# Kernel optimization log

Measured on AMD Instinct MI355X. Metric: run time of the kernel, lower is better.

## Reference

```python
import jax, jax.numpy as jnp
import numpy as np

B, CIN, H, W = 16, 3, 224, 224
COUT = 128
EPS = 1e-5  # BatchNorm2d default eps


def setup_inputs() -> dict:
    key = jax.random.key(0)
    ks = jax.random.split(key, 7)
    x = jax.random.normal(ks[0], (B, CIN, H, W), dtype=jnp.float32)
    conv_w = jax.random.normal(ks[1], (COUT, CIN, 7, 7), dtype=jnp.float32) * 0.05
    conv_b = jax.random.normal(ks[2], (COUT,), dtype=jnp.float32) * 0.05
    bn_gamma = 1.0 + 0.1 * jax.random.normal(ks[3], (COUT,), dtype=jnp.float32)
    bn_beta = 0.05 * jax.random.normal(ks[4], (COUT,), dtype=jnp.float32)
    bn_mean = 0.1 * jax.random.normal(ks[5], (COUT,), dtype=jnp.float32)
    bn_var = jax.random.uniform(ks[6], (COUT,), dtype=jnp.float32, minval=0.5, maxval=1.5)
    return {"x": x, "conv_w": conv_w, "conv_b": conv_b, "bn_gamma": bn_gamma,
            "bn_beta": bn_beta, "bn_mean": bn_mean, "bn_var": bn_var}


def reference(x, conv_w, conv_b, bn_gamma, bn_beta, bn_mean, bn_var):
    b = x.shape[0]
    # Conv2d 3->128, k7, stride 1, pad 3  -> [B,128,H,W]
    y = jax.lax.conv_general_dilated(
        x, conv_w, window_strides=(1, 1), padding=[(3, 3), (3, 3)],
        dimension_numbers=("NCHW", "OIHW", "NCHW"))
    y = y + conv_b[None, :, None, None]
    # BatchNorm2d (inference form with running stats), then ReLU
    scale = bn_gamma * jax.lax.rsqrt(bn_var + EPS)
    y = (y - bn_mean[None, :, None, None]) * scale[None, :, None, None] + bn_beta[None, :, None, None]
    y = jax.nn.relu(y)
    h, w = y.shape[2], y.shape[3]
    # channel-last, top-3 over channels -> [B,H,W,3]
    y_cl = jnp.transpose(y, (0, 2, 3, 1))
    top3, idx3 = jax.lax.top_k(y_cl, 3)
    # MaxPool3d kernel (3,1,1) over the top-3 axis of [B,3,H,W]: max of the 3
    # sorted top-k values == top3[..., 0]. Flatten spatial -> [B,1,H*W]
    max_vals = top3[..., 0].reshape(b, 1, h * w)
    _, idx = jax.lax.top_k(max_vals, 128)  # idx: [B,1,128] flat spatial indices
    # flatten top3/idx3 to [B,3,H*W] (channel-first layout, matching torch transposes)
    top3_f = jnp.transpose(top3, (0, 3, 1, 2)).reshape(b, 3, h * w)
    idx3_f = jnp.transpose(idx3, (0, 3, 1, 2)).reshape(b, 3, h * w)
    gidx = jnp.broadcast_to(idx, (b, 3, 128))
    reduced_top3 = jnp.take_along_axis(top3_f, gidx, axis=2)              # [B,3,128]
    reduced_idx3 = jnp.take_along_axis(idx3_f, gidx, axis=2).astype(jnp.float32)
    return reduced_idx3, reduced_top3, idx
```

## Files before the change

kernel.cpp:

```cpp
#include <hip/hip_runtime.h>
#include <math.h>

#define BATCH 16
#define CIN   3
#define HH    224
#define WW    224
#define HW    (HH*WW)
#define COUT  128
#define TAPS  147
#define CAND  192
#define TK    192

typedef __attribute__((ext_vector_type(8))) _Float16 f16x8_t;
typedef decltype(__builtin_amdgcn_cvt_pkrtz(0.f, 0.f)) f16x2_t;
typedef __attribute__((ext_vector_type(4))) float f32x4_t;
typedef __attribute__((ext_vector_type(16))) float f32x16_t;
typedef __attribute__((ext_vector_type(4))) unsigned int u32x4_t;
typedef unsigned long long u64;
typedef unsigned int u32;

#define B_CHUNKS  (24*129)
#define B_BYTES   (B_CHUNKS*16u)
#define CPY_STRIDE 2192
#define CPY_BYTES  (8*CPY_STRIDE)
#define XFSTR     25
#define XF_OFF    (B_BYTES + CPY_BYTES)
#define LBSH_OFF  (XF_OFF + 6656u)
#define PMAX_OFF  (LBSH_OFF + 512u)
#define LHIST_OFF (PMAX_OFF + 1024u)
#define LDS_CONV  (LHIST_OFF + 4096u)

#define WS_BG    0u
#define WS_BSH   (WS_BG + B_BYTES)
#define WS_TOP1  (WS_BSH + 512u)
#define WS_CIDX  (WS_TOP1 + (unsigned)(BATCH*HW*4))
#define WS_CKEY  (WS_CIDX + (unsigned)(BATCH*CAND*4))
#define WS_C3V   (WS_CKEY + (unsigned)(BATCH*CAND*8))
#define WS_C3I   (WS_C3V + (unsigned)(BATCH*CAND*3*4))
#define WS_WT    (WS_C3I + (unsigned)(BATCH*CAND*3*4))
#define WS_HIST  (WS_WT + (unsigned)(TAPS*COUT*4))
#define ZERO_N   (BATCH*1024)

__device__ __forceinline__ void gload_lds16(const u32* g, u32* l) {
  __builtin_amdgcn_global_load_lds((const __attribute__((address_space(1))) u32*)g,
                                   (__attribute__((address_space(3))) u32*)l, 16, 0, 0);
}

__global__ void prep_kernel(const float* __restrict__ w, const float* __restrict__ cb,
                            const float* __restrict__ gamma, const float* __restrict__ beta,
                            const float* __restrict__ mean, const float* __restrict__ var,
                            unsigned short* __restrict__ Bg, float* __restrict__ bsh,
                            float* __restrict__ wT, u32* __restrict__ gh) {
  int c = blockIdx.x;
  int t = threadIdx.x;
  int zi = c*192 + t;
  if (zi < ZERO_N) gh[zi] = 0u;
  float s = gamma[c] * (1.0f / sqrtf(var[c] + 1e-5f));
  int g = t >> 3, kw = t & 7;
  float wraw = 0.0f;
  if (g < 21 && kw < 7) {
    wraw = w[c*TAPS + g*7 + kw];
    wT[(g*7 + kw)*COUT + c] = wraw;
  }
  union { _Float16 h; unsigned short u; } cvt;
  cvt.h = (_Float16)(wraw * s);
  Bg[((g*129 + c)*8) + kw] = cvt.u;
  if (t == 0) bsh[c] = (cb[c] - mean[c]) * s + beta[c];
}

__global__ __launch_bounds__(512, 4)
void conv_mfma_kernel(const float* __restrict__ x, const unsigned short* __restrict__ Bg,
                      const float* __restrict__ bsh, float* __restrict__ top1,
                      u32* __restrict__ gh) {
  extern __shared__ char smem[];
  char* xcop = smem + B_BYTES;
  float* xf   = (float*)(smem + XF_OFF);
  float* lbsh = (float*)(smem + LBSH_OFF);
  float* pmax = (float*)(smem + PMAX_OFF);
  u32* lhist  = (u32*)(smem + LHIST_OFF);

  int tid = threadIdx.x;
  int lane = tid & 63, wv = tid >> 6;
  int p = lane & 31, kh2 = lane >> 5;
  int chp = wv & 1, pxp = wv >> 1;
  int b = blockIdx.z, w0 = blockIdx.x*16, h0 = blockIdx.y*16;
  const float* xb = x + (size_t)b * CIN * HW;
  const u32* Bg32 = (const u32*)Bg;

#pragma unroll
  for (int k = 0; k < 7; ++k) {
    int idx = tid + k*512;
    if (idx < B_CHUNKS) gload_lds16(Bg32 + idx*4, (u32*)smem + idx*4);
  }
  for (int i = tid; i < CIN*22*24; i += 512) {
    int cin = i / (22*24);
    int rem = i % (22*24);
    int r = rem / 24, col = rem % 24;
    int gh2 = h0 + r - 3, gw = w0 + col - 3;
    float v = 0.0f;
    if (gh2 >= 0 && gh2 < HH && gw >= 0 && gw < WW) v = xb[cin*HW + gh2*WW + gw];
    xf[(cin*22 + r)*XFSTR + col] = v;
  }
  if (tid < COUT) lbsh[tid] = bsh[tid];
  for (int i = tid; i < 1024; i += 512) lhist[i] = 0u;

  __syncthreads();

  for (int c = tid; c < 8*132; c += 512) {
    int s   = c / 132;
    int rem = c % 132;
    int cin = rem / 44;
    int rm2 = rem % 44;
    int r   = rm2 >> 1, cj = rm2 & 1;
    const float* src = xf + (cin*22 + r)*XFSTR + 8*cj + s;
    float xv[8];
#pragma unroll
    for (int j = 0; j < 8; ++j) xv[j] = src[j];
    union { f16x2_t pk[4]; u32x4_t v; } P;
#pragma unroll
    for (int j = 0; j < 4; ++j)
      P.pk[j] = __builtin_amdgcn_cvt_pkrtz(xv[2*j], xv[2*j+1]);
    *(u32x4_t*)(xcop + s*CPY_STRIDE + (cin*22 + r)*32 + cj*16) = P.v;
  }

  __syncthreads();

  f32x16_t acc[2][2];
#pragma unroll
  for (int i = 0; i < 2; ++i)
#pragma unroll
    for (int j = 0; j < 2; ++j)
#pragma unroll
      for (int r = 0; r < 16; ++r) acc[i][j][r] = 0.0f;

  const f16x8_t* B8 = (const f16x8_t*)smem;
  int lane_base = (p & 7)*CPY_STRIDE + ((p >> 3) & 1)*16;
  const char* xl = xcop + lane_base;
  int prow = p >> 4;

#pragma unroll
  for (int kf = 0; kf < 12; ++kf) {
    int g = kf*2 + kh2;
    f16x8_t Wn[2];
#pragma unroll
    for (int i = 0; i < 2; ++i)
      Wn[i] = B8[g*129 + chp*64 + i*32 + p];
    int cin = (g*37) >> 8;
    int kh = g - cin*7;
    int rowb = (g < 21) ? (cin*22 + kh) : 0;
#pragma unroll
    for (int j = 0; j < 2; ++j) {
      int pxrow = pxp*4 + j*2 + prow;
      f16x8_t Av = *(const f16x8_t*)(xl + (rowb + pxrow)*32);
#pragma unroll
      for (int i = 0; i < 2; ++i)
        acc[i][j] = __builtin_amdgcn_mfma_f32_32x32x16_f16(Wn[i], Av, acc[i][j], 0, 0, 0);
    }
  }

  f32x4_t bvv[2][4];
#pragma unroll
  for (int i = 0; i < 2; ++i)
#pragma unroll
    for (int gq = 0; gq < 4; ++gq)
      bvv[i][gq] = *(const f32x4_t*)(lbsh + chp*64 + i*32 + gq*8 + kh2*4);

  float vm[2];
#pragma unroll
  for (int j = 0; j < 2; ++j) {
    float v = -1e30f;
#pragma unroll
    for (int i = 0; i < 2; ++i)
#pragma unroll
      for (int gq = 0; gq < 4; ++gq)
#pragma unroll
        for (int t = 0; t < 4; ++t)
          v = fmaxf(v, acc[i][j][gq*4 + t] + bvv[i][gq][t]);
    v = fmaxf(v, __shfl_xor(v, 32));
    vm[j] = v;
  }
  if (chp == 0 && lane < 32) {
#pragma unroll
    for (int j = 0; j < 2; ++j) pmax[pxp*64 + j*32 + p] = vm[j];
  }
  __syncthreads();
  if (chp == 1 && lane < 32) {
#pragma unroll
    for (int j = 0; j < 2; ++j) {
      int px = pxp*64 + j*32 + p;
      float r = fmaxf(fmaxf(vm[j], pmax[px]), 0.0f);
      top1[(size_t)b*HW + (h0 + (px >> 4))*WW + (w0 + (px & 15))] = r;
      atomicAdd(&lhist[__float_as_uint(r) >> 21], 1u);
    }
  }
  __syncthreads();
  for (int i = tid; i < 1024; i += 512) {
    u32 cv = lhist[i];
    if (cv) atomicAdd(&gh[b*1024 + i], cv);
  }
}

#define SNT 1024
__global__ void select_kernel(const float* __restrict__ top1, const u32* __restrict__ gh,
                              int* __restrict__ cand) {
  int img = blockIdx.x, tid = threadIdx.x;
  const float* v = top1 + (size_t)img * HW;
  const float4* v4 = (const float4*)v;
  __shared__ u32 hist[1024];
  __shared__ u64 keys[1024];
  __shared__ unsigned sG, scnt, sbin, sthr, snc;

  hist[tid] = gh[img*1024 + tid];
  __syncthreads();
  if (tid < 64) {
    int j = tid;
    unsigned s = 0;
#pragma unroll
    for (int i = 0; i < 16; ++i) s += hist[j*16 + i];
    unsigned a = s;
#pragma unroll
    for (int d = 1; d < 64; d <<= 1) { unsigned t = __shfl_down(a, d); if (j + d < 64) a += t; }
    unsigned above = a - s;
    if (above < TK && a >= TK) {
      unsigned cum = above;
      for (int i = 15; i >= 0; --i) {
        unsigned c = hist[j*16 + i];
        if (cum + c >= TK) { sG = cum; scnt = c; sbin = (unsigned)(j*16 + i); break; }
        cum += c;
      }
    }
    if (j == 0 && a < TK) { sG = 0; scnt = hist[0]; sbin = 0; }
  }
  __syncthreads();
  unsigned G = sG, cnt = scnt, binT = sbin;
  unsigned thr = binT << 21;
  if (G + cnt > 1024u) {
    __syncthreads();
    hist[tid] = 0u;
    __syncthreads();
    for (int i = tid; i < HW/4; i += SNT) {
      float4 f = v4[i];
      float fv[4] = {f.x, f.y, f.z, f.w};
#pragma unroll
      for (int c = 0; c < 4; ++c) {
        unsigned ub = __float_as_uint(fv[c]);
        if ((ub >> 21) == binT) atomicAdd(&hist[(ub >> 11) & 0x3FFu], 1u);
      }
    }
    __syncthreads();
    unsigned TK2 = TK - G;
    if (tid < 64) {
      int j = tid;
      unsigned s = 0;
#pragma unroll
      for (int i = 0; i < 16; ++i) s += hist[j*16 + i];
      unsigned a = s;
#pragma unroll
      for (int d = 1; d < 64; d <<= 1) { unsigned t = __shfl_down(a, d); if (j + d < 64) a += t; }
      unsigned above = a - s;
      if (above < TK2 && a >= TK2) {
        unsigned cum = above;
        for (int i = 15; i >= 0; --i) {
          unsigned c = hist[j*16 + i];
          if (cum + c >= TK2) { sthr = (binT << 21) | ((unsigned)(j*16 + i) << 11); break; }
          cum += c;
        }
      }
      if (j == 0 && a < TK2) sthr = binT << 21;
    }
    __syncthreads();
    thr = sthr;
  }
  if (tid == 0) snc = 0u;
  keys[tid] = 0ull;
  __syncthreads();
  for (int i = tid; i < HW/4; i += SNT) {
    float4 f = v4[i];
    float fv[4] = {f.x, f.y, f.z, f.w};
#pragma unroll
    for (int c = 0; c < 4; ++c) {
      unsigned ub = __float_as_uint(fv[c]);
      if (ub >= thr) {
        unsigned pp = atomicAdd(&snc, 1u);
        if (pp < 1024u) keys[pp] = ((u64)ub << 32) | (unsigned)(~(unsigned)(4*i + c));
      }
    }
  }
  for (unsigned kk = 2; kk <= 1024; kk <<= 1)
    for (unsigned j = kk >> 1; j > 0; j >>= 1) {
      __syncthreads();
      unsigned t = tid, ixj = t ^ j;
      if (ixj > t) {
        u64 a = keys[t], b = keys[ixj];
        bool desc = ((t & kk) == 0);
        if ((a < b) == desc) { keys[t] = b; keys[ixj] = a; }
      }
    }
  __syncthreads();
  if (tid < CAND) {
    u64 key = keys[tid];
    cand[img*CAND + tid] = (key == 0ull) ? -1 : (int)(~(unsigned)(key & 0xFFFFFFFFull));
  }
}

__global__ void refine_kernel(const float* __restrict__ x, const float* __restrict__ wT,
                              const float* __restrict__ cb, const float* __restrict__ gamma,
                              const float* __restrict__ beta, const float* __restrict__ mean,
                              const float* __restrict__ var, const int* __restrict__ cand,
                              u64* __restrict__ ckey,
                              float* __restrict__ c3v, float* __restrict__ c3i) {
#pragma clang fp contract(off)
  int slot = blockIdx.x, img = blockIdx.y;
  int c = threadIdx.x;
  int sidx = cand[img*CAND + slot];
  if (sidx < 0) {
    if (c == 0) {
      ckey[img*CAND + slot] = 0ull;
      for (int j = 0; j < 3; ++j) { c3v[(img*CAND+slot)*3+j] = 0.f; c3i[(img*CAND+slot)*3+j] = 0.f; }
    }
    return;
  }
  int h = sidx / WW, wq = sidx % WW;
  const float* xb = x + (size_t)img * CIN * HW;

  __shared__ float xs[TAPS + 13];
  for (int t = c; t < TAPS; t += 128) {
    int cin = t / 49, r = t % 49;
    int kh = r / 7, kw = r % 7;
    int gh = h - 3 + kh, gw = wq - 3 + kw;
    float v = 0.0f;
    if (gh >= 0 && gh < HH && gw >= 0 && gw < WW) v = xb[cin*HW + gh*WW + gw];
    xs[t] = v;
  }
  __syncthreads();

  double acc = 0.0;
#pragma unroll 7
  for (int t = 0; t < TAPS; ++t)
    acc = fma((double)xs[t], (double)wT[t*COUT + c], acc);

  float y = (float)acc;
  y = y + cb[c];
  float s  = gamma[c] * (1.0f / sqrtf(var[c] + 1e-5f));
  float t1 = (y - mean[c]) * s;
  float z  = t1 + beta[c];
  z = fmaxf(z, 0.0f);

  __shared__ u64 zk[COUT];
  zk[c] = ((u64)__float_as_uint(z) << 32) | (unsigned)(127 - c);
  __syncthreads();
  if (c < 64) {
    u64 k0 = zk[c], k1 = zk[c + 64];
    int base = (img*CAND + slot)*3;
#pragma unroll
    for (int pick = 0; pick < 3; ++pick) {
      u64 m = (k0 > k1) ? k0 : k1;
#pragma unroll
      for (int d = 1; d < 64; d <<= 1) {
        u64 o = __shfl_xor((unsigned long long)m, d);
        if (o > m) m = o;
      }
      if (c == 0) {
        c3v[base + pick] = __uint_as_float((unsigned)(m >> 32));
        c3i[base + pick] = (float)(127 - (int)(m & 0xFFFFFFFFull));
        if (pick == 0)
          ckey[img*CAND + slot] = ((u64)(m >> 32) << 32) | (unsigned)(~(unsigned)sidx);
      }
      if (k0 == m) k0 = 0ull;
      if (k1 == m) k1 = 0ull;
    }
  }
}

__global__ void final_kernel(const u64* __restrict__ ckey, const int* __restrict__ cand,
                             const float* __restrict__ c3v, const float* __restrict__ c3i,
                             float* __restrict__ out) {
  int img = blockIdx.x, tid = threadIdx.x;
  __shared__ u64 k[256];
  __shared__ int pay[256];
  k[tid]  = (tid < CAND) ? ckey[img*CAND + tid] : 0ull;
  pay[tid] = tid;
  for (unsigned kk = 2; kk <= 256; kk <<= 1)
    for (unsigned j = kk >> 1; j > 0; j >>= 1) {
      __syncthreads();
      unsigned i = tid, ixj = i ^ j;
      if (ixj > i) {
        u64 a = k[i], b = k[ixj];
        bool desc = ((i & kk) == 0);
        if ((a < b) == desc) {
          k[i] = b; k[ixj] = a;
          int p = pay[i]; pay[i] = pay[ixj]; pay[ixj] = p;
        }
      }
    }
  __syncthreads();
  if (tid < 128) {
    int slot = pay[tid];
    int sidx = cand[img*CAND + slot];
    out[12288 + img*128 + tid] = (float)sidx;
    int base = (img*CAND + slot)*3;
    for (int j = 0; j < 3; ++j) {
      out[(img*3 + j)*128 + tid]        = c3i[base + j];
      out[6144 + (img*3 + j)*128 + tid] = c3v[base + j];
    }
  }
}

extern "C" void kernel_launch(void* const* d_in, const int* in_sizes, int n_in,
                              void* d_out, int out_size, void* d_ws, size_t ws_size,
                              hipStream_t stream) {
  const float* x     = (const float*)d_in[0];
  const float* w     = (const float*)d_in[1];
  const float* cb    = (const float*)d_in[2];
  const float* gamma = (const float*)d_in[3];
  const float* beta  = (const float*)d_in[4];
  const float* mean  = (const float*)d_in[5];
  const float* var   = (const float*)d_in[6];
  float* out = (float*)d_out;
  char*  ws  = (char*)d_ws;

  unsigned short* Bg = (unsigned short*)(ws + WS_BG);
  float* bsh  = (float*)(ws + WS_BSH);
  float* top1 = (float*)(ws + WS_TOP1);
  int*   cidx = (int*)(ws + WS_CIDX);
  u64*   ck   = (u64*)(ws + WS_CKEY);
  float* c3v = (float*)(ws + WS_C3V);
  float* c3i = (float*)(ws + WS_C3I);
  float* wT  = (float*)(ws + WS_WT);
  u32* gh    = (u32*)(ws + WS_HIST);

  prep_kernel<<<COUT, 192, 0, stream>>>(w, cb, gamma, beta, mean, var, Bg, bsh, wT, gh);
  conv_mfma_kernel<<<dim3(WW/16, HH/16, BATCH), 512, LDS_CONV, stream>>>(x, Bg, bsh, top1, gh);
  select_kernel<<<BATCH, SNT, 0, stream>>>(top1, gh, cidx);
  refine_kernel<<<dim3(CAND, BATCH), COUT, 0, stream>>>(x, wT, cb, gamma, beta, mean, var,
                                                        cidx, ck, c3v, c3i);
  final_kernel<<<BATCH, 256, 0, stream>>>(ck, cidx, c3v, c3i, out);
}
```

Before: 94.00 us.

## Halve conv weight LDS footprint by loading weights in two phases

The conv kernel now keeps only half of the fp16 weight tiles in LDS at a time and reloads the second half between two MFMA passes. The histogram buffer is aliased onto the fp32 input staging area once that area is dead. Together these shrink per-block LDS so more blocks can be resident per CU. In exchange, each block adds two barriers and a mid-kernel global-to-LDS load that cannot overlap with compute.

Result: no change. 94.43 us (+0.4%).

```diff
diff --git a/kernel.cpp b/kernel.cpp
--- a/kernel.cpp
+++ b/kernel.cpp
@@ -19,19 +19,20 @@
 typedef unsigned long long u64;
 typedef unsigned int u32;
 
-#define B_CHUNKS  (24*129)
-#define B_BYTES   (B_CHUNKS*16u)
+#define B_CHUNKS   (24*129)
+#define BH_CHUNKS  (12*129)
+#define BH_BYTES   (BH_CHUNKS*16u)
 #define CPY_STRIDE 2192
 #define CPY_BYTES  (8*CPY_STRIDE)
 #define XFSTR     25
-#define XF_OFF    (B_BYTES + CPY_BYTES)
+#define XCOP_OFF  BH_BYTES
+#define XF_OFF    (XCOP_OFF + CPY_BYTES)
 #define LBSH_OFF  (XF_OFF + 6656u)
 #define PMAX_OFF  (LBSH_OFF + 512u)
-#define LHIST_OFF (PMAX_OFF + 1024u)
-#define LDS_CONV  (LHIST_OFF + 4096u)
+#define LDS_CONV  (PMAX_OFF + 1024u)
 
 #define WS_BG    0u
-#define WS_BSH   (WS_BG + B_BYTES)
+#define WS_BSH   (WS_BG + (unsigned)(B_CHUNKS*16))
 #define WS_TOP1  (WS_BSH + 512u)
 #define WS_CIDX  (WS_TOP1 + (unsigned)(BATCH*HW*4))
 #define WS_CKEY  (WS_CIDX + (unsigned)(BATCH*CAND*4))
@@ -73,11 +74,11 @@
                       const float* __restrict__ bsh, float* __restrict__ top1,
                       u32* __restrict__ gh) {
   extern __shared__ char smem[];
-  char* xcop = smem + B_BYTES;
+  char* xcop  = smem + XCOP_OFF;
   float* xf   = (float*)(smem + XF_OFF);
+  u32* lhist  = (u32*)(smem + XF_OFF);
   float* lbsh = (float*)(smem + LBSH_OFF);
   float* pmax = (float*)(smem + PMAX_OFF);
-  u32* lhist  = (u32*)(smem + LHIST_OFF);
 
   int tid = threadIdx.x;
   int lane = tid & 63, wv = tid >> 6;
@@ -88,9 +89,9 @@
   const u32* Bg32 = (const u32*)Bg;
 
 #pragma unroll
-  for (int k = 0; k < 7; ++k) {
+  for (int k = 0; k < 4; ++k) {
     int idx = tid + k*512;
-    if (idx < B_CHUNKS) gload_lds16(Bg32 + idx*4, (u32*)smem + idx*4);
+    if (idx < BH_CHUNKS) gload_lds16(Bg32 + idx*4, (u32*)smem + idx*4);
   }
   for (int i = tid; i < CIN*22*24; i += 512) {
     int cin = i / (22*24);
@@ -102,7 +103,6 @@
     xf[(cin*22 + r)*XFSTR + col] = v;
   }
   if (tid < COUT) lbsh[tid] = bsh[tid];
-  for (int i = tid; i < 1024; i += 512) lhist[i] = 0u;
 
   __syncthreads();
 
@@ -125,6 +125,8 @@
 
   __syncthreads();
 
+  for (int i = tid; i < 1024; i += 512) lhist[i] = 0u;
+
   f32x16_t acc[2][2];
 #pragma unroll
   for (int i = 0; i < 2; ++i)
@@ -139,22 +141,35 @@
   int prow = p >> 4;
 
 #pragma unroll
-  for (int kf = 0; kf < 12; ++kf) {
-    int g = kf*2 + kh2;
-    f16x8_t Wn[2];
-#pragma unroll
-    for (int i = 0; i < 2; ++i)
-      Wn[i] = B8[g*129 + chp*64 + i*32 + p];
-    int cin = (g*37) >> 8;
-    int kh = g - cin*7;
-    int rowb = (g < 21) ? (cin*22 + kh) : 0;
-#pragma unroll
-    for (int j = 0; j < 2; ++j) {
-      int pxrow = pxp*4 + j*2 + prow;
-      f16x8_t Av = *(const f16x8_t*)(xl + (rowb + pxrow)*32);
+  for (int half = 0; half < 2; ++half) {
+    if (half == 1) {
+      __syncthreads();
+#pragma unroll
+      for (int k = 0; k < 4; ++k) {
+        int idx = tid + k*512;
+        if (idx < BH_CHUNKS) gload_lds16(Bg32 + (BH_CHUNKS + idx)*4, (u32*)smem + idx*4);
+      }
+      __syncthreads();
+    }
+#pragma unroll
+    for (int kfl = 0; kfl < 6; ++kfl) {
+      int glo = kfl*2 + kh2;
+      int g = half*12 + glo;
+      f16x8_t Wn[2];
 #pragma unroll
       for (int i = 0; i < 2; ++i)
-        acc[i][j] = __builtin_amdgcn_mfma_f32_32x32x16_f16(Wn[i], Av, acc[i][j], 0, 0, 0);
+        Wn[i] = B8[glo*129 + chp*64 + i*32 + p];
+      int cin = (g*37) >> 8;
+      int kh = g - cin*7;
+      int rowb = (g < 21) ? (cin*22 + kh) : 0;
+#pragma unroll
+      for (int j = 0; j < 2; ++j) {
+        int pxrow = pxp*4 + j*2 + prow;
+        f16x8_t Av = *(const f16x8_t*)(xl + (rowb + pxrow)*32);
+#pragma unroll
+        for (int i = 0; i < 2; ++i)
+          acc[i][j] = __builtin_amdgcn_mfma_f32_32x32x16_f16(Wn[i], Av, acc[i][j], 0, 0, 0);
+      }
     }
   }
 
```
